# Optimization experiments

Hardware: AMD Instinct MI355X
Metric: run time of the kernel (lower is better)

Reference implementation:

```python
import jax, jax.numpy as jnp
import numpy as np
from jax import lax

IH, IW = 32, 32
N = IH * IW
C = 256
HEADS = 8
DH = C // HEADS
SCALE = 32 ** -0.5  # uses dim_head arg (32), as in the torch module
EPS = 1e-6


def _rel_index():
    coords = np.stack(np.meshgrid(np.arange(IH), np.arange(IW), indexing='ij')).reshape(2, -1)
    rel = coords[:, :, None] - coords[:, None, :]  # [2, n, n]
    rel[0] += IH - 1
    rel[1] += IW - 1
    rel[0] *= 2 * IW - 1
    return jnp.asarray(rel.sum(0).reshape(-1))  # [n*n] int

REL_IDX = _rel_index()


def _conv3(x, W):
    # 3x3 conv, stride 1, pad 1, no bias; NCHW / OIHW
    return lax.conv_general_dilated(x, W, (1, 1), 'SAME',
                                    dimension_numbers=('NCHW', 'OIHW', 'NCHW'))


def _proj(x, W, g, b):
    # conv3x3 -> GroupNorm(1 group, per-channel affine) -> exact GELU -> split heads
    y = _conv3(x, W)
    m = jnp.mean(y, axis=(1, 2, 3), keepdims=True)
    v = jnp.var(y, axis=(1, 2, 3), keepdims=True)
    y = (y - m) * lax.rsqrt(v + EPS) * g[None, :, None, None] + b[None, :, None, None]
    y = jax.nn.gelu(y, approximate=False)
    B = y.shape[0]
    # b c h w -> b (h d heads split) : channel c = head*DH + d  -> b h n d
    return y.reshape(B, HEADS, DH, N).transpose(0, 1, 3, 2)


def setup_inputs() -> dict:
    key = jax.random.key(0)
    ks = jax.random.split(key, 8)
    s = 0.02
    return {
        'x': jax.random.normal(ks[0], (8, C, IH, IW), dtype=jnp.float32),
        'Wq': jax.random.normal(ks[1], (C, C, 3, 3), dtype=jnp.float32) * s,
        'gq': jnp.ones((C,), jnp.float32), 'bq': jnp.zeros((C,), jnp.float32),
        'Wk': jax.random.normal(ks[2], (C, C, 3, 3), dtype=jnp.float32) * s,
        'gk': jnp.ones((C,), jnp.float32), 'bk': jnp.zeros((C,), jnp.float32),
        'Wv': jax.random.normal(ks[3], (C, C, 3, 3), dtype=jnp.float32) * s,
        'gv': jnp.ones((C,), jnp.float32), 'bv': jnp.zeros((C,), jnp.float32),
        'bias_table': jax.random.normal(ks[4], ((2 * IH - 1) * (2 * IW - 1), HEADS), dtype=jnp.float32) * s,
        'Wout': jax.random.normal(ks[5], (C, C, 1, 1), dtype=jnp.float32) * s,
        'bout': jnp.zeros((C,), jnp.float32),
    }


def reference(x, Wq, gq, bq, Wk, gk, bk, Wv, gv, bv, bias_table, Wout, bout):
    B = x.shape[0]
    q = _proj(x, Wq, gq, bq)  # [B, H, N, DH]
    k = _proj(x, Wk, gk, bk)
    v = _proj(x, Wv, gv, bv)
    dots = jnp.einsum('bhnd,bhmd->bhnm', q, k) * SCALE  # [B, H, N, N]
    # gather relative position bias: [n*n, heads] -> [1, heads, n, n]
    bias = bias_table[REL_IDX].reshape(N, N, HEADS).transpose(2, 0, 1)[None]
    attn = jax.nn.softmax(dots + bias, axis=-1)
    out = jnp.einsum('bhnm,bhmd->bhnd', attn, v)  # [B, H, N, DH]
    # b h n d -> b n (h d) -> b c ih iw
    out = out.transpose(0, 2, 1, 3).reshape(B, N, C).transpose(0, 2, 1).reshape(B, C, IH, IW)
    # 1x1 conv projection with bias (Dropout2d is identity at eval)
    out = jnp.einsum('oc,bchw->bohw', Wout[:, :, 0, 0], out) + bout[None, :, None, None]
    return out
```

## Files before the change

kernel.cpp:

```cpp
#include <hip/hip_runtime.h>

typedef float f32x4 __attribute__((ext_vector_type(4)));
typedef short bf16x8 __attribute__((ext_vector_type(8)));
typedef short bf16x4 __attribute__((ext_vector_type(4)));

#define PADN 1156

typedef const __attribute__((address_space(1))) void* gptr_t;
typedef __attribute__((address_space(3))) void* lptr_t;

__device__ __forceinline__ short f2b(float f) {
  unsigned u = __float_as_uint(f);
  unsigned r = (u + 0x7FFFu + ((u >> 16) & 1u)) >> 16;
  return (short)r;
}
__device__ __forceinline__ float b2f(short s) {
  return __uint_as_float(((unsigned)(unsigned short)s) << 16);
}

__global__ __launch_bounds__(256) void prep(const float* __restrict__ x,
                                            const float* __restrict__ Wq,
                                            const float* __restrict__ Wk,
                                            const float* __restrict__ Wv,
                                            const float* __restrict__ Wout,
                                            short* __restrict__ xpad,
                                            short* __restrict__ wpack,
                                            short* __restrict__ woutp) {
  __shared__ float lds[2304];
  int blk0 = blockIdx.x;
  int t = threadIdx.x;
  if (blk0 < 2048) {
    int wg = blk0;
    int b = wg >> 8, rem = wg & 255;
    int cb = rem >> 5, sb = rem & 31;
    int sl = t & 31, cq = t >> 5;
    const float* xb = x + ((b * 256 + cb * 32) * 1024) + sb * 32;
#pragma unroll
    for (int i = 0; i < 4; i++) {
      int cl = cq + i * 8;
      lds[cl * 33 + sl] = xb[cl * 1024 + sl];
    }
    __syncthreads();
    int cl2 = t & 31, sq = t >> 5;
    short* xp = xpad + b * (PADN * 256) + cb * 32 + cl2;
#pragma unroll
    for (int i = 0; i < 4; i++) {
      int sl2 = sq + i * 8;
      int s = sb * 32 + sl2;
      int pidx = ((s >> 5) + 1) * 34 + (s & 31) + 1;
      xp[pidx * 256] = f2b(lds[cl2 * 33 + sl2]);
    }
  } else {
    int blk = blk0 - 2048;
    if (blk < 768) {
      int p = blk >> 8, o = blk & 255;
      const float* W = (p == 0) ? Wq : (p == 1) ? Wk : Wv;
      const float* src = W + o * 2304;
      for (int i = t; i < 2304; i += 256) lds[i] = src[i];
      __syncthreads();
      short* dst = wpack + p * 589824 + o * 2304;
#pragma unroll
      for (int tt = 0; tt < 9; tt++) dst[tt * 256 + t] = f2b(lds[t * 9 + tt]);
    } else {
      int e = (blk - 768) * 1024 + t * 4;
      f32x4 v = *(const f32x4*)(Wout + e);
      bf16x4 o4;
#pragma unroll
      for (int j = 0; j < 4; j++) o4[j] = f2b(v[j]);
      *(bf16x4*)(woutp + e) = o4;
    }
  }
}

__global__ __launch_bounds__(256, 2) void conv_gemm(const short* __restrict__ xpad,
                                                    const short* __restrict__ wpack,
                                                    short* __restrict__ qn,
                                                    short* __restrict__ kn,
                                                    short* __restrict__ vn,
                                                    float* __restrict__ stats,
                                                    const float* __restrict__ btab,
                                                    short* __restrict__ biasP) {
  __shared__ short ldsA[2][8192];
  __shared__ short ldsB[2][8192];
  int bid = blockIdx.x;
  int tid = threadIdx.x;
  if (bid >= 384) {
    const float L2E = 1.4426950408889634f;
#pragma unroll
    for (int it = 0; it < 4; it++) {
      int id = (bid - 384) * 1024 + it * 256 + tid;
      int lane = id & 63;
      int rest = id >> 6;
      int jt = rest & 3; rest >>= 2;
      int kb = rest & 15; rest >>= 4;
      int qblk = rest & 63; rest >>= 6;
      int h = rest;
      int li = lane & 15, g = lane >> 4;
      int qrow = qblk * 16 + li;
      int yi = qrow >> 5, xi = qrow & 31;
      int ibase = (yi + 31) * 63 + (xi + 31);
      int j0 = kb * 64 + jt * 16 + g * 4;
      int yj = j0 >> 5, xj0 = j0 & 31;
      int idx0 = ibase - yj * 63 - xj0;
      bf16x4 v;
#pragma unroll
      for (int rr = 0; rr < 4; rr++) v[rr] = f2b(btab[(idx0 - rr) * 8 + h] * L2E);
      *(bf16x4*)(biasP + (size_t)id * 4) = v;
    }
    return;
  }
  int wg = (bid & 7) * 48 + (bid >> 3);
  int b = wg / 48;
  int rr0 = wg - b * 48;
  int p = (rr0 < 16) ? 0 : (rr0 < 32) ? 1 : 2;
  int t16 = rr0 & 15;
  bool xA = (p < 2);
  int mt_i = xA ? (t16 >> 1) : (t16 >> 3);
  int nt_i = xA ? (t16 & 1) : (t16 & 7);
  int m0 = mt_i * 128, n0 = nt_i * 128;
  int lane = tid & 63, wave = tid >> 6;
  int wr = wave >> 1, wc = wave & 1;
  int g = lane >> 4, li = lane & 15;

  const char* xb = (const char*)(xpad + b * (PADN * 256));
  const char* wp = (const char*)(wpack + p * (256 * 2304));
  const char* abase = xA ? xb : wp;
  const char* bbase = xA ? wp : xb;

  int srow = tid >> 3;
  int schunk = ((tid & 7) ^ (srow & 7)) * 16;
  int aoff[4], boff[4];
#pragma unroll
  for (int q = 0; q < 4; q++) {
    int row = m0 + q * 32 + srow;
    aoff[q] = (xA ? ((((row >> 5) + 1) * 34 + (row & 31) + 1) * 512) : (row * 4608)) + schunk;
  }
#pragma unroll
  for (int q = 0; q < 4; q++) {
    int row = n0 + q * 32 + srow;
    boff[q] = (xA ? (row * 4608) : ((((row >> 5) + 1) * 34 + (row & 31) + 1) * 512)) + schunk;
  }

  int aadr[4][2], badr[4][2];
#pragma unroll
  for (int mt = 0; mt < 4; mt++) {
    int row = wr * 64 + mt * 16 + li;
#pragma unroll
    for (int ksub = 0; ksub < 2; ksub++)
      aadr[mt][ksub] = row * 64 + (((ksub * 4 + g) ^ (row & 7)) * 8);
  }
#pragma unroll
  for (int nt = 0; nt < 4; nt++) {
    int row = wc * 64 + nt * 16 + li;
#pragma unroll
    for (int ksub = 0; ksub < 2; ksub++)
      badr[nt][ksub] = row * 64 + (((ksub * 4 + g) ^ (row & 7)) * 8);
  }

#define STAGE(KS, BUF) do {                                                        \
    int t_ = (KS) >> 2, cq_ = (KS) & 3;                                            \
    int ty_ = (t_ * 11) >> 5;                                                      \
    int doff_ = (ty_ - 1) * 34 + (t_ - 3 * ty_) - 1;                               \
    int kA_ = (xA ? doff_ * 512 : t_ * 512) + cq_ * 128;                           \
    int kB_ = (xA ? t_ * 512 : doff_ * 512) + cq_ * 128;                           \
    _Pragma("unroll")                                                              \
    for (int q_ = 0; q_ < 4; q_++)                                                 \
      __builtin_amdgcn_global_load_lds((gptr_t)(abase + aoff[q_] + kA_),           \
                                       (lptr_t)&ldsA[BUF][(q_ * 256 + tid) * 8],   \
                                       16, 0, 0);                                  \
    _Pragma("unroll")                                                              \
    for (int q_ = 0; q_ < 4; q_++)                                                 \
      __builtin_amdgcn_global_load_lds((gptr_t)(bbase + boff[q_] + kB_),           \
                                       (lptr_t)&ldsB[BUF][(q_ * 256 + tid) * 8],   \
                                       16, 0, 0);                                  \
  } while (0)

  f32x4 acc[4][4] = {};
  STAGE(0, 0);
  __syncthreads();
#pragma unroll 2
  for (int ks = 0; ks < 36; ks++) {
    int cur = ks & 1;
    if (ks < 35) STAGE(ks + 1, cur ^ 1);
    bf16x8 af[4][2], bfv[4][2];
#pragma unroll
    for (int mt = 0; mt < 4; mt++)
#pragma unroll
      for (int ksub = 0; ksub < 2; ksub++)
        af[mt][ksub] = *(const bf16x8*)&ldsA[cur][aadr[mt][ksub]];
#pragma unroll
    for (int nt = 0; nt < 4; nt++)
#pragma unroll
      for (int ksub = 0; ksub < 2; ksub++)
        bfv[nt][ksub] = *(const bf16x8*)&ldsB[cur][badr[nt][ksub]];
#pragma unroll
    for (int ksub = 0; ksub < 2; ksub++)
#pragma unroll
      for (int mt = 0; mt < 4; mt++)
#pragma unroll
        for (int nt = 0; nt < 4; nt++)
          acc[mt][nt] = __builtin_amdgcn_mfma_f32_16x16x32_bf16(af[mt][ksub], bfv[nt][ksub], acc[mt][nt], 0, 0, 0);
    __syncthreads();
  }
#undef STAGE

  short* outp = (p == 0) ? qn : (p == 1) ? kn : vn;
  int ostride = xA ? 256 : 1024;
  int obase = b * 262144;
  float s1 = 0.f, s2 = 0.f;
#pragma unroll
  for (int mt = 0; mt < 4; mt++)
#pragma unroll
    for (int nt = 0; nt < 4; nt++) {
      int col = n0 + wc * 64 + nt * 16 + li;
#pragma unroll
      for (int rr = 0; rr < 4; rr++) {
        int row = m0 + wr * 64 + mt * 16 + g * 4 + rr;
        float v = acc[mt][nt][rr];
        s1 += v;
        s2 += v * v;
        outp[obase + row * ostride + col] = f2b(v);
      }
    }
#pragma unroll
  for (int off = 1; off < 64; off <<= 1) {
    s1 += __shfl_xor(s1, off);
    s2 += __shfl_xor(s2, off);
  }
  if (lane == 0) {
    atomicAdd(&stats[(b * 3 + p) * 2], s1);
    atomicAdd(&stats[(b * 3 + p) * 2 + 1], s2);
  }
}

__global__ __launch_bounds__(256) void norm_gelu(const short* __restrict__ qn, const short* __restrict__ kn,
                                                 const short* __restrict__ vn,
                                                 short* __restrict__ qpk, short* __restrict__ kpk,
                                                 short* __restrict__ vpk,
                                                 const float* __restrict__ stats,
                                                 const float* __restrict__ gq, const float* __restrict__ bq,
                                                 const float* __restrict__ gk, const float* __restrict__ bk,
                                                 const float* __restrict__ gv, const float* __restrict__ bv) {
  long e = ((long)blockIdx.x * 256 + threadIdx.x) * 8;
  int buf = (int)(e >> 21);
  int w = (int)(e & 2097151);
  int b = w >> 18;
  int pos = w & 262143;
  const short* base = (buf == 0) ? qn : (buf == 1) ? kn : vn;
  const float* gg = (buf == 0) ? gq : (buf == 1) ? gk : gv;
  const float* bb = (buf == 0) ? bq : (buf == 1) ? bk : bv;
  float s1 = stats[(b * 3 + buf) * 2];
  float s2 = stats[(b * 3 + buf) * 2 + 1];
  float mean = s1 * (1.f / 262144.f);
  float var = s2 * (1.f / 262144.f) - mean * mean;
  float rstd = rsqrtf(var + 1e-6f);
  const float PS = 0.17677669529663687f * 1.4426950408889634f;
  float post = (buf == 0) ? PS : 1.f;
  bf16x8 v = *(const bf16x8*)(base + (size_t)b * 262144 + pos);
#pragma unroll
  for (int j = 0; j < 8; j++) {
    int ch = (buf < 2) ? ((pos + j) & 255) : ((pos + j) >> 10);
    float y = b2f(v[j]);
    y = (y - mean) * rstd * gg[ch] + bb[ch];
    y = 0.5f * y * (1.f + erff(y * 0.70710678118f));
    v[j] = f2b(y * post);
  }
  if (buf < 2) {
    int s = pos >> 8, c = pos & 255;
    int h2 = c >> 5, g2 = (c >> 3) & 3;
    short* dst = (buf == 0) ? qpk : kpk;
    size_t addr = ((size_t)((b * 8 + h2) * 64 + (s >> 4))) * 512 + (g2 * 16 + (s & 15)) * 8;
    *(bf16x8*)(dst + addr) = v;
  } else {
    int c = pos >> 10, s0 = pos & 1023;
    int h2 = c >> 5, d = c & 31;
    int dblk = d >> 4, liv = d & 15;
    int kv32 = s0 >> 5, jr0 = s0 & 31;
    int hi = jr0 >> 4, g0 = (jr0 >> 2) & 3;
    size_t addr = ((size_t)((b * 8 + h2) * 32 + kv32) * 2 + dblk) * 512 + hi * 4 + liv * 8;
    bf16x4 lo4 = {v[0], v[1], v[2], v[3]};
    bf16x4 hi4 = {v[4], v[5], v[6], v[7]};
    *(bf16x4*)(vpk + addr + g0 * 128) = lo4;
    *(bf16x4*)(vpk + addr + (g0 + 1) * 128) = hi4;
  }
}

__global__ __launch_bounds__(256, 4) void attn(const short* __restrict__ qpk,
                                               const short* __restrict__ kpk,
                                               const short* __restrict__ vpk,
                                               const short* __restrict__ biasP,
                                               short* __restrict__ obuf) {
  int wg = blockIdx.x;
  int b = wg >> 7, rem = wg & 127;
  int h = rem >> 4, qt = rem & 15;
  int lane = threadIdx.x & 63, wave = threadIdx.x >> 6;
  int g = lane >> 4, li = lane & 15;
  int qblk = qt * 4 + wave;
  int qbase = qblk * 16;
  const short* qpb = qpk + ((size_t)((b * 8 + h) * 64 + qblk)) * 512;
  const short* kpb = kpk + ((size_t)((b * 8 + h) * 64)) * 512;
  const short* vpb = vpk + ((size_t)(b * 8 + h)) * 32768;
  const short* bpb = biasP + (((size_t)(h * 64 + qblk)) << 14) + lane * 4;
  bf16x8 qf = *(const bf16x8*)(qpb + lane * 8);
  float m = -1e30f, l = 0.f;
  f32x4 oacc[2] = {};
  bf16x8 kf[4];
  bf16x4 bfr[4];
#pragma unroll
  for (int jt = 0; jt < 4; jt++) {
    kf[jt] = *(const bf16x8*)(kpb + jt * 512 + lane * 8);
    bfr[jt] = *(const bf16x4*)(bpb + jt * 256);
  }
#pragma unroll 1
  for (int kb = 0; kb < 16; kb++) {
    f32x4 st[4];
#pragma unroll
    for (int jt = 0; jt < 4; jt++) {
      f32x4 cinit;
#pragma unroll
      for (int rr = 0; rr < 4; rr++) cinit[rr] = b2f(bfr[jt][rr]);
      st[jt] = __builtin_amdgcn_mfma_f32_16x16x32_bf16(kf[jt], qf, cinit, 0, 0, 0);
    }
    bf16x8 kf2[4];
    bf16x4 bfr2[4];
    if (kb < 15) {
#pragma unroll
      for (int jt = 0; jt < 4; jt++) {
        kf2[jt] = *(const bf16x8*)(kpb + ((kb + 1) * 4 + jt) * 512 + lane * 8);
        bfr2[jt] = *(const bf16x4*)(bpb + (kb + 1) * 1024 + jt * 256);
      }
    }
    bf16x8 vf[2][2];
#pragma unroll
    for (int nt = 0; nt < 2; nt++)
#pragma unroll
      for (int ks = 0; ks < 2; ks++)
        vf[nt][ks] = *(const bf16x8*)(vpb + ((kb * 2 + ks) * 2 + nt) * 512 + lane * 8);
    float mb = -1e30f;
#pragma unroll
    for (int jt = 0; jt < 4; jt++)
#pragma unroll
      for (int rr = 0; rr < 4; rr++) mb = fmaxf(mb, st[jt][rr]);
    mb = fmaxf(mb, __shfl_xor(mb, 16));
    mb = fmaxf(mb, __shfl_xor(mb, 32));
    if (!__all(mb <= m + 8.f)) {
      float mnew = fmaxf(m, mb);
      float alpha = exp2f(m - mnew);
      m = mnew;
      l *= alpha;
#pragma unroll
      for (int rr = 0; rr < 4; rr++) {
        float ar = __shfl(alpha, (lane & 0x30) | (g * 4 + rr));
        oacc[0][rr] *= ar;
        oacc[1][rr] *= ar;
      }
    }
    float ls = 0.f;
    bf16x8 pf0, pf1;
#pragma unroll
    for (int jt = 0; jt < 4; jt++)
#pragma unroll
      for (int rr = 0; rr < 4; rr++) {
        float pe = exp2f(st[jt][rr] - m);
        ls += pe;
        int q2 = jt * 4 + rr;
        if (q2 < 8) pf0[q2] = f2b(pe); else pf1[q2 - 8] = f2b(pe);
      }
    ls += __shfl_xor(ls, 16);
    ls += __shfl_xor(ls, 32);
    l += ls;
#pragma unroll
    for (int nt = 0; nt < 2; nt++)
#pragma unroll
      for (int ks = 0; ks < 2; ks++)
        oacc[nt] = __builtin_amdgcn_mfma_f32_16x16x32_bf16(ks == 0 ? pf0 : pf1, vf[nt][ks], oacc[nt], 0, 0, 0);
    if (kb < 15) {
#pragma unroll
      for (int jt = 0; jt < 4; jt++) {
        kf[jt] = kf2[jt];
        bfr[jt] = bfr2[jt];
      }
    }
  }
  float linv = 1.f / l;
  short* ob = obuf + (b * 1024) * 256 + h * 32;
#pragma unroll
  for (int rr = 0; rr < 4; rr++) {
    float lr = __shfl(linv, (lane & 0x30) | (g * 4 + rr));
    int row = qbase + g * 4 + rr;
    ob[row * 256 + li] = f2b(oacc[0][rr] * lr);
    ob[row * 256 + 16 + li] = f2b(oacc[1][rr] * lr);
  }
}

__global__ __launch_bounds__(256) void out_gemm(const short* __restrict__ woutp,
                                                const short* __restrict__ obuf,
                                                const float* __restrict__ bout,
                                                float* __restrict__ out) {
  int wg = blockIdx.x;
  int b = wg >> 5, rem = wg & 31;
  int mt_i = rem >> 4, nt_i = rem & 15;
  int m0 = mt_i * 128, n0 = nt_i * 64;
  int lane = threadIdx.x & 63, wave = threadIdx.x >> 6;
  int wr = wave >> 1, wc = wave & 1;
  int g = lane >> 4, li = lane & 15;
  int aoff[4];
#pragma unroll
  for (int mt = 0; mt < 4; mt++) aoff[mt] = (m0 + wr * 64 + mt * 16 + li) * 256;
  int boff[2];
#pragma unroll
  for (int nt = 0; nt < 2; nt++) boff[nt] = (b * 1024 + n0 + wc * 32 + nt * 16 + li) * 256;
  f32x4 acc[4][2] = {};
#pragma unroll
  for (int ks = 0; ks < 8; ks++) {
    int kof = ks * 32 + g * 8;
    bf16x8 af[4], bfr[2];
#pragma unroll
    for (int mt = 0; mt < 4; mt++) af[mt] = *(const bf16x8*)(woutp + aoff[mt] + kof);
#pragma unroll
    for (int nt = 0; nt < 2; nt++) bfr[nt] = *(const bf16x8*)(obuf + boff[nt] + kof);
#pragma unroll
    for (int mt = 0; mt < 4; mt++)
#pragma unroll
      for (int nt = 0; nt < 2; nt++)
        acc[mt][nt] = __builtin_amdgcn_mfma_f32_16x16x32_bf16(af[mt], bfr[nt], acc[mt][nt], 0, 0, 0);
  }
#pragma unroll
  for (int mt = 0; mt < 4; mt++)
#pragma unroll
    for (int nt = 0; nt < 2; nt++) {
      int col = n0 + wc * 32 + nt * 16 + li;
#pragma unroll
      for (int rr = 0; rr < 4; rr++) {
        int row = m0 + wr * 64 + mt * 16 + g * 4 + rr;
        out[b * 262144 + row * 1024 + col] = acc[mt][nt][rr] + bout[row];
      }
    }
}

extern "C" void kernel_launch(void* const* d_in, const int* in_sizes, int n_in,
                              void* d_out, int out_size, void* d_ws, size_t ws_size,
                              hipStream_t stream) {
  const float* x = (const float*)d_in[0];
  const float* Wq = (const float*)d_in[1];
  const float* gq = (const float*)d_in[2];
  const float* bq = (const float*)d_in[3];
  const float* Wk = (const float*)d_in[4];
  const float* gk = (const float*)d_in[5];
  const float* bk = (const float*)d_in[6];
  const float* Wv = (const float*)d_in[7];
  const float* gv = (const float*)d_in[8];
  const float* bv = (const float*)d_in[9];
  const float* btab = (const float*)d_in[10];
  const float* Wout = (const float*)d_in[11];
  const float* bout = (const float*)d_in[12];
  float* out = (float*)d_out;

  char* ws = (char*)d_ws;
  size_t off = 0;
  float* stats = (float*)(ws + off); off += 256;
  short* xpad = (short*)(ws + off); off += (size_t)8 * PADN * 256 * 2;
  short* wpack = (short*)(ws + off); off += (size_t)3 * 256 * 2304 * 2;
  short* woutp = (short*)(ws + off); off += (size_t)256 * 256 * 2;
  short* qn = (short*)(ws + off); off += (size_t)4194304;
  short* kn = (short*)(ws + off); off += (size_t)4194304;
  short* vn = (short*)(ws + off); off += (size_t)4194304;
  short* obuf = (short*)(ws + off); off += (size_t)4194304;
  short* qpk = (short*)(ws + off); off += (size_t)4194304;
  short* kpk = (short*)(ws + off); off += (size_t)4194304;
  short* vpk = (short*)(ws + off); off += (size_t)4194304;
  short* biasP = (short*)(ws + off); off += (size_t)8 * 1024 * 1024 * 2;
  if (ws_size < off) return;

  hipMemsetAsync(stats, 0, 256, stream);
  hipMemsetAsync(xpad, 0, (size_t)8 * PADN * 256 * 2, stream);
  prep<<<2880, 256, 0, stream>>>(x, Wq, Wk, Wv, Wout, xpad, wpack, woutp);
  conv_gemm<<<2432, 256, 0, stream>>>(xpad, wpack, qn, kn, vn, stats, btab, biasP);
  norm_gelu<<<3072, 256, 0, stream>>>(qn, kn, vn, qpk, kpk, vpk, stats, gq, bq, gk, bk, gv, bv);
  attn<<<1024, 256, 0, stream>>>(qpk, kpk, vpk, biasP, obuf);
  out_gemm<<<256, 256, 0, stream>>>(woutp, obuf, bout, out);
}
```

Before: 141.8 us.

## Split attention key range across two waves and merge softmax partials in LDS

After: 294.5 us. 2.08x slower.

```diff
diff --git a/kernel.cpp b/kernel.cpp
--- a/kernel.cpp
+++ b/kernel.cpp
@@ -285,18 +285,21 @@
   }
 }
 
-__global__ __launch_bounds__(256, 4) void attn(const short* __restrict__ qpk,
+__global__ __launch_bounds__(256, 6) void attn(const short* __restrict__ qpk,
                                                const short* __restrict__ kpk,
                                                const short* __restrict__ vpk,
                                                const short* __restrict__ biasP,
                                                short* __restrict__ obuf) {
+  __shared__ float part[2][64][10];
   int wg = blockIdx.x;
-  int b = wg >> 7, rem = wg & 127;
-  int h = rem >> 4, qt = rem & 15;
+  int b = wg >> 8, rem = wg & 255;
+  int h = rem >> 5, qt2 = rem & 31;
   int lane = threadIdx.x & 63, wave = threadIdx.x >> 6;
+  int qlocal = wave >> 1, half = wave & 1;
   int g = lane >> 4, li = lane & 15;
-  int qblk = qt * 4 + wave;
+  int qblk = qt2 * 2 + qlocal;
   int qbase = qblk * 16;
+  int kb0 = half * 8;
   const short* qpb = qpk + ((size_t)((b * 8 + h) * 64 + qblk)) * 512;
   const short* kpb = kpk + ((size_t)((b * 8 + h) * 64)) * 512;
   const short* vpb = vpk + ((size_t)(b * 8 + h)) * 32768;
@@ -308,11 +311,11 @@
   bf16x4 bfr[4];
 #pragma unroll
   for (int jt = 0; jt < 4; jt++) {
-    kf[jt] = *(const bf16x8*)(kpb + jt * 512 + lane * 8);
-    bfr[jt] = *(const bf16x4*)(bpb + jt * 256);
+    kf[jt] = *(const bf16x8*)(kpb + (kb0 * 4 + jt) * 512 + lane * 8);
+    bfr[jt] = *(const bf16x4*)(bpb + kb0 * 1024 + jt * 256);
   }
 #pragma unroll 1
-  for (int kb = 0; kb < 16; kb++) {
+  for (int kb = kb0; kb < kb0 + 8; kb++) {
     f32x4 st[4];
 #pragma unroll
     for (int jt = 0; jt < 4; jt++) {
@@ -323,7 +326,7 @@
     }
     bf16x8 kf2[4];
     bf16x4 bfr2[4];
-    if (kb < 15) {
+    if (kb < kb0 + 7) {
 #pragma unroll
       for (int jt = 0; jt < 4; jt++) {
         kf2[jt] = *(const bf16x8*)(kpb + ((kb + 1) * 4 + jt) * 512 + lane * 8);
@@ -374,7 +377,7 @@
 #pragma unroll
       for (int ks = 0; ks < 2; ks++)
         oacc[nt] = __builtin_amdgcn_mfma_f32_16x16x32_bf16(ks == 0 ? pf0 : pf1, vf[nt][ks], oacc[nt], 0, 0, 0);
-    if (kb < 15) {
+    if (kb < kb0 + 7) {
 #pragma unroll
       for (int jt = 0; jt < 4; jt++) {
         kf[jt] = kf2[jt];
@@ -382,14 +385,34 @@
       }
     }
   }
-  float linv = 1.f / l;
-  short* ob = obuf + (b * 1024) * 256 + h * 32;
-#pragma unroll
-  for (int rr = 0; rr < 4; rr++) {
-    float lr = __shfl(linv, (lane & 0x30) | (g * 4 + rr));
-    int row = qbase + g * 4 + rr;
-    ob[row * 256 + li] = f2b(oacc[0][rr] * lr);
-    ob[row * 256 + 16 + li] = f2b(oacc[1][rr] * lr);
+  if (half == 1) {
+#pragma unroll
+    for (int rr = 0; rr < 4; rr++) {
+      part[qlocal][lane][rr] = oacc[0][rr];
+      part[qlocal][lane][4 + rr] = oacc[1][rr];
+    }
+    part[qlocal][lane][8] = m;
+    part[qlocal][lane][9] = l;
+  }
+  __syncthreads();
+  if (half == 0) {
+    short* ob = obuf + (b * 1024) * 256 + h * 32;
+#pragma unroll
+    for (int rr = 0; rr < 4; rr++) {
+      int rl = (lane & 0x30) | (g * 4 + rr);
+      float m_r = __shfl(m, rl);
+      float l_r = __shfl(l, rl);
+      float mb_r = part[qlocal][rl][8];
+      float lb_r = part[qlocal][rl][9];
+      float M = fmaxf(m_r, mb_r);
+      float wa = exp2f(m_r - M), wb = exp2f(mb_r - M);
+      float inv = 1.f / (l_r * wa + lb_r * wb);
+      float o0 = (oacc[0][rr] * wa + part[qlocal][lane][rr] * wb) * inv;
+      float o1 = (oacc[1][rr] * wa + part[qlocal][lane][4 + rr] * wb) * inv;
+      int row = qbase + g * 4 + rr;
+      ob[row * 256 + li] = f2b(o0);
+      ob[row * 256 + 16 + li] = f2b(o1);
+    }
   }
 }
 
@@ -477,6 +500,6 @@
   prep<<<2880, 256, 0, stream>>>(x, Wq, Wk, Wv, Wout, xpad, wpack, woutp);
   conv_gemm<<<2432, 256, 0, stream>>>(xpad, wpack, qn, kn, vn, stats, btab, biasP);
   norm_gelu<<<3072, 256, 0, stream>>>(qn, kn, vn, qpk, kpk, vpk, stats, gq, bq, gk, bk, gv, bv);
-  attn<<<1024, 256, 0, stream>>>(qpk, kpk, vpk, biasP, obuf);
+  attn<<<2048, 256, 0, stream>>>(qpk, kpk, vpk, biasP, obuf);
   out_gemm<<<256, 256, 0, stream>>>(woutp, obuf, bout, out);
 }
```

## Stage K/V tiles through double-buffered LDS via direct global-to-LDS loads

Applied to the files above, without the earlier changes.

New measurement: 144.4 us. Within noise of the previous version (+1.8%).

```diff
diff --git a/kernel.cpp b/kernel.cpp
--- a/kernel.cpp
+++ b/kernel.cpp
@@ -290,60 +290,61 @@
                                                const short* __restrict__ vpk,
                                                const short* __restrict__ biasP,
                                                short* __restrict__ obuf) {
+  __shared__ short ldsK[2][2048];
+  __shared__ short ldsV[2][2048];
   int wg = blockIdx.x;
   int b = wg >> 7, rem = wg & 127;
-  int h = rem >> 4, qt = rem & 15;
-  int lane = threadIdx.x & 63, wave = threadIdx.x >> 6;
+  int h = rem >> 4, qt4 = rem & 15;
+  int tid = threadIdx.x;
+  int lane = tid & 63, wave = tid >> 6;
   int g = lane >> 4, li = lane & 15;
-  int qblk = qt * 4 + wave;
+  int qblk = qt4 * 4 + wave;
   int qbase = qblk * 16;
   const short* qpb = qpk + ((size_t)((b * 8 + h) * 64 + qblk)) * 512;
-  const short* kpb = kpk + ((size_t)((b * 8 + h) * 64)) * 512;
-  const short* vpb = vpk + ((size_t)(b * 8 + h)) * 32768;
+  const char* kpc = (const char*)(kpk + ((size_t)((b * 8 + h) * 64)) * 512);
+  const char* vpc = (const char*)(vpk + ((size_t)(b * 8 + h)) * 32768);
   const short* bpb = biasP + (((size_t)(h * 64 + qblk)) << 14) + lane * 4;
   bf16x8 qf = *(const bf16x8*)(qpb + lane * 8);
   float m = -1e30f, l = 0.f;
   f32x4 oacc[2] = {};
-  bf16x8 kf[4];
   bf16x4 bfr[4];
 #pragma unroll
-  for (int jt = 0; jt < 4; jt++) {
-    kf[jt] = *(const bf16x8*)(kpb + jt * 512 + lane * 8);
-    bfr[jt] = *(const bf16x4*)(bpb + jt * 256);
-  }
+  for (int jt = 0; jt < 4; jt++) bfr[jt] = *(const bf16x4*)(bpb + jt * 256);
+  __builtin_amdgcn_global_load_lds((gptr_t)(kpc + tid * 16), (lptr_t)&ldsK[0][tid * 8], 16, 0, 0);
+  __builtin_amdgcn_global_load_lds((gptr_t)(vpc + tid * 16), (lptr_t)&ldsV[0][tid * 8], 16, 0, 0);
+  __syncthreads();
 #pragma unroll 1
   for (int kb = 0; kb < 16; kb++) {
+    int cur = kb & 1;
+    if (kb < 15) {
+      __builtin_amdgcn_global_load_lds((gptr_t)(kpc + (kb + 1) * 4096 + tid * 16),
+                                       (lptr_t)&ldsK[cur ^ 1][tid * 8], 16, 0, 0);
+      __builtin_amdgcn_global_load_lds((gptr_t)(vpc + (kb + 1) * 4096 + tid * 16),
+                                       (lptr_t)&ldsV[cur ^ 1][tid * 8], 16, 0, 0);
+    }
     f32x4 st[4];
 #pragma unroll
     for (int jt = 0; jt < 4; jt++) {
+      bf16x8 kf = *(const bf16x8*)&ldsK[cur][jt * 512 + lane * 8];
       f32x4 cinit;
 #pragma unroll
       for (int rr = 0; rr < 4; rr++) cinit[rr] = b2f(bfr[jt][rr]);
-      st[jt] = __builtin_amdgcn_mfma_f32_16x16x32_bf16(kf[jt], qf, cinit, 0, 0, 0);
-    }
-    bf16x8 kf2[4];
+      st[jt] = __builtin_amdgcn_mfma_f32_16x16x32_bf16(kf, qf, cinit, 0, 0, 0);
+    }
     bf16x4 bfr2[4];
     if (kb < 15) {
 #pragma unroll
-      for (int jt = 0; jt < 4; jt++) {
-        kf2[jt] = *(const bf16x8*)(kpb + ((kb + 1) * 4 + jt) * 512 + lane * 8);
+      for (int jt = 0; jt < 4; jt++)
         bfr2[jt] = *(const bf16x4*)(bpb + (kb + 1) * 1024 + jt * 256);
-      }
-    }
-    bf16x8 vf[2][2];
-#pragma unroll
-    for (int nt = 0; nt < 2; nt++)
-#pragma unroll
-      for (int ks = 0; ks < 2; ks++)
-        vf[nt][ks] = *(const bf16x8*)(vpb + ((kb * 2 + ks) * 2 + nt) * 512 + lane * 8);
-    float mb = -1e30f;
+    }
+    float mbl = -1e30f;
 #pragma unroll
     for (int jt = 0; jt < 4; jt++)
 #pragma unroll
-      for (int rr = 0; rr < 4; rr++) mb = fmaxf(mb, st[jt][rr]);
-    mb = fmaxf(mb, __shfl_xor(mb, 16));
-    mb = fmaxf(mb, __shfl_xor(mb, 32));
-    if (!__all(mb <= m + 8.f)) {
+      for (int rr = 0; rr < 4; rr++) mbl = fmaxf(mbl, st[jt][rr]);
+    if (!__all(mbl <= m + 8.f)) {
+      float mb = fmaxf(mbl, __shfl_xor(mbl, 16));
+      mb = fmaxf(mb, __shfl_xor(mb, 32));
       float mnew = fmaxf(m, mb);
       float alpha = exp2f(m - mnew);
       m = mnew;
@@ -366,22 +367,22 @@
         int q2 = jt * 4 + rr;
         if (q2 < 8) pf0[q2] = f2b(pe); else pf1[q2 - 8] = f2b(pe);
       }
-    ls += __shfl_xor(ls, 16);
-    ls += __shfl_xor(ls, 32);
     l += ls;
 #pragma unroll
     for (int nt = 0; nt < 2; nt++)
 #pragma unroll
-      for (int ks = 0; ks < 2; ks++)
-        oacc[nt] = __builtin_amdgcn_mfma_f32_16x16x32_bf16(ks == 0 ? pf0 : pf1, vf[nt][ks], oacc[nt], 0, 0, 0);
+      for (int ks = 0; ks < 2; ks++) {
+        bf16x8 vf = *(const bf16x8*)&ldsV[cur][(ks * 2 + nt) * 512 + lane * 8];
+        oacc[nt] = __builtin_amdgcn_mfma_f32_16x16x32_bf16(ks == 0 ? pf0 : pf1, vf, oacc[nt], 0, 0, 0);
+      }
     if (kb < 15) {
 #pragma unroll
-      for (int jt = 0; jt < 4; jt++) {
-        kf[jt] = kf2[jt];
-        bfr[jt] = bfr2[jt];
-      }
-    }
-  }
+      for (int jt = 0; jt < 4; jt++) bfr[jt] = bfr2[jt];
+    }
+    __syncthreads();
+  }
+  l += __shfl_xor(l, 16);
+  l += __shfl_xor(l, 32);
   float linv = 1.f / l;
   short* ob = obuf + (b * 1024) * 256 + h * 32;
 #pragma unroll
```
